# Kernel optimization log

Hardware: AMD Instinct MI355X
Metric: run time of the kernel (lower is better)

The kernel has to match this reference:

```python
import jax, jax.numpy as jnp
from jax import lax
import numpy as np

H = 128; L = 4; N_TOTAL = 4096; M = 4; S = 16384; K = 12; SK = S * K
MAX_DIST = 32; B = 64; NH = 4; DH = H // NH; BN_EPS = 1e-5


def _bn(x, g, b):
    # training-mode BatchNorm1d over rows (biased variance)
    mu = x.mean(0)
    var = x.var(0)
    return (x - mu) * lax.rsqrt(var + BN_EPS) * g + b


def _gine(x, src, dst, ea, eps, We, bWe, W1, b1, W2, b2):
    # PyG GINEConv: mlp((1+eps)*x + sum_j relu(x_j + lin(e_ji)))
    msg = jax.nn.relu(x[src] + ea @ We.T + bWe)
    agg = jax.ops.segment_sum(msg, dst, num_segments=x.shape[0])
    h = (1.0 + eps) * x + agg
    return jax.nn.relu(h @ W1.T + b1) @ W2.T + b2


def _forward(log_probs, atom_tab, bond_tab, dist_tab, logp_W, logp_b, lw, lb,
             bn_g, bn_b, eps, mha_in_W, mha_in_b, mha_out_W, mha_out_b, ro_g, ro_b,
             atom_ids, node_ids, intra_ei, intra_bond_ids, edge_index, canon_bond_ids, batch):
    sub_batch = jnp.arange(SK, dtype=jnp.int32) // K
    root_flat = jnp.arange(S, dtype=jnp.int32) * K
    valid_f = (node_ids >= 0).astype(jnp.float32)[:, None]
    clamped = jnp.maximum(node_ids, 0)
    x_flat = atom_tab[atom_ids][clamped]            # [SK, H]
    ea_flat = bond_tab[intra_bond_ids]              # [E_intra, H]
    edge_attr = bond_tab[canon_bond_ids]            # [E_canon, H]
    src, dst = intra_ei[0], intra_ei[1]

    # BFS distances from subgraph roots (min-plus relaxation, MAX_DIST sweeps)
    d0 = jnp.full((SK,), MAX_DIST, jnp.int32).at[root_flat].set(0)
    dist = lax.fori_loop(0, MAX_DIST, lambda i, d: d.at[dst].min(d[src] + 1), d0)
    dist = jnp.minimum(dist, MAX_DIST)
    dist_pe = dist_tab[dist]

    logp_pe = jax.nn.relu(log_probs[sub_batch][:, None] @ logp_W.T + logp_b)
    h = (x_flat + dist_pe + logp_pe) * valid_f

    is_root_f = jnp.zeros((SK, 1), jnp.float32).at[root_flat].set(1.0)
    root_ids = node_ids[root_flat]                  # canonical id of each root (>=0)
    cnt = jnp.maximum(jax.ops.segment_sum(jnp.ones((S,), jnp.float32), root_ids,
                                          num_segments=N_TOTAL), 1.0)

    for l in range(L):
        W = lw[l]; bv = lb[l]
        h1 = _gine(h, src, dst, ea_flat, eps[l, 0], W[0], bv[0], W[1], bv[1], W[2], bv[2])
        h1 = _bn(h1, bn_g[l, 0], bn_b[l, 0]) * valid_f
        h_root_b = h[sub_batch * K]
        h_nr = h @ W[3].T + bv[3] + h_root_b @ W[4].T + bv[4]
        h_can = jax.ops.segment_sum(h[root_flat], root_ids, num_segments=N_TOTAL) / cnt[:, None]
        h_int = _gine(h_can, edge_index[0], edge_index[1], edge_attr, eps[l, 1],
                      W[5], bv[5], W[6], bv[6], W[7], bv[7])
        h_int = _bn(h_int, bn_g[l, 1], bn_b[l, 1])
        h_ib = h_int[clamped] * valid_f
        out = is_root_f * (h1 + h_ib) + (1.0 - is_root_f) * (h1 + h_nr)
        h = jax.nn.relu(out) * valid_f

    # subgraph sum-pool (invalid rows are zeroed so scatter of zeros is a no-op)
    h_sub = jax.ops.segment_sum(h * valid_f, sub_batch, num_segments=S)
    order = jnp.argsort(root_ids)                   # stable by default
    h2 = h_sub[order].reshape(N_TOTAL, M, H)

    # MultiheadAttention over the m subgraphs of each canonical node
    qkv = h2 @ mha_in_W.T + mha_in_b
    q, k_, v = jnp.split(qkv, 3, axis=-1)
    hd = lambda t: t.reshape(N_TOTAL, M, NH, DH).transpose(0, 2, 1, 3)
    q, k_, v = hd(q), hd(k_), hd(v)
    scale = np.float32(1.0 / np.sqrt(DH))
    attn = jax.nn.softmax(jnp.einsum('nhqd,nhkd->nhqk', q, k_) * scale, axis=-1)
    o = jnp.einsum('nhqk,nhkd->nhqd', attn, v).transpose(0, 2, 1, 3).reshape(N_TOTAL, M, H)
    h_attn = o @ mha_out_W.T + mha_out_b + h2
    node_emb = _bn(h_attn.mean(1), ro_g, ro_b)
    return jax.ops.segment_sum(node_emb, batch, num_segments=B)


def setup_inputs() -> dict:
    key = jax.random.key(0)
    ks = jax.random.split(key, 32)
    rn = lambda i, sh, sc=0.1: (jax.random.normal(ks[i], sh) * sc).astype(jnp.float32)
    atom_ids = jax.random.randint(ks[0], (N_TOTAL,), 0, 64, dtype=jnp.int32)
    nid = jax.random.randint(ks[1], (S, K), 0, N_TOTAL, dtype=jnp.int32)
    pad = jax.random.uniform(ks[2], (S, K)) < 0.1
    nid = jnp.where(pad, -1, nid)
    nid = nid.at[:, 0].set(jnp.arange(S, dtype=jnp.int32) // M)  # roots: each canonical node m times
    node_ids = nid.reshape(-1)
    flat = jnp.arange(SK, dtype=jnp.int32).reshape(S, K)
    intra_ei = jnp.stack([flat[:, :-1].reshape(-1), flat[:, 1:].reshape(-1)])  # chains per subgraph
    intra_bond_ids = jax.random.randint(ks[3], (S * (K - 1),), 0, 8, dtype=jnp.int32)
    edge_index = jax.random.randint(ks[4], (2, N_TOTAL * 8), 0, N_TOTAL, dtype=jnp.int32)
    canon_bond_ids = jax.random.randint(ks[5], (N_TOTAL * 8,), 0, 8, dtype=jnp.int32)
    batch = jnp.arange(N_TOTAL, dtype=jnp.int32) // (N_TOTAL // B)
    log_probs = jax.random.normal(ks[6], (S,), dtype=jnp.float32)
    return dict(
        atom_ids=atom_ids, node_ids=node_ids, intra_ei=intra_ei,
        intra_bond_ids=intra_bond_ids, edge_index=edge_index,
        canon_bond_ids=canon_bond_ids, batch=batch, log_probs=log_probs,
        atom_tab=rn(7, (64, H)), bond_tab=rn(8, (8, H)), dist_tab=rn(9, (MAX_DIST + 1, H)),
        logp_W=rn(10, (H, 1)), logp_b=jnp.zeros((H,), jnp.float32),
        lw=rn(11, (L, 8, H, H)), lb=jnp.zeros((L, 8, H), jnp.float32),
        bn_g=jnp.ones((L, 2, H), jnp.float32), bn_b=jnp.zeros((L, 2, H), jnp.float32),
        eps=jnp.zeros((L, 2), jnp.float32),
        mha_in_W=rn(12, (3 * H, H)), mha_in_b=jnp.zeros((3 * H,), jnp.float32),
        mha_out_W=rn(13, (H, H)), mha_out_b=jnp.zeros((H,), jnp.float32),
        ro_g=jnp.ones((H,), jnp.float32), ro_b=jnp.zeros((H,), jnp.float32))


def reference(atom_ids, node_ids, intra_ei, intra_bond_ids, edge_index, canon_bond_ids,
              batch, log_probs, atom_tab, bond_tab, dist_tab, logp_W, logp_b, lw, lb,
              bn_g, bn_b, eps, mha_in_W, mha_in_b, mha_out_W, mha_out_b, ro_g, ro_b):
    return _forward(log_probs, atom_tab, bond_tab, dist_tab, logp_W, logp_b, lw, lb,
                    bn_g, bn_b, eps, mha_in_W, mha_in_b, mha_out_W, mha_out_b, ro_g, ro_b,
                    atom_ids, node_ids, intra_ei, intra_bond_ids, edge_index, canon_bond_ids, batch)
```

## Files before the change

### kernel.cpp

```cpp
#include <hip/hip_runtime.h>
#include <math.h>

#define DEV static __device__ __forceinline__

constexpr int H    = 128;
constexpr int Ksub = 12;
constexpr int S    = 16384;
constexpr int SK   = S * Ksub;
constexpr int NTOT = 4096;

typedef __attribute__((ext_vector_type(8))) short bhalf8;
typedef __attribute__((ext_vector_type(4))) float floatx4;

DEV float4 ld4(const float* p) { return *(const float4*)p; }
DEV void   st4(float* p, float4 v) { *(float4*)p = v; }

DEV ushort f2b(float f) {
  unsigned x = __float_as_uint(f);
  return (ushort)((x + 0x7FFFu + ((x >> 16) & 1u)) >> 16);
}
DEV float b2f(ushort u) { return __uint_as_float(((unsigned)u) << 16); }

DEV void split8(const float* v, bhalf8& hi, bhalf8& lo) {
#pragma unroll
  for (int j = 0; j < 8; ++j) {
    ushort hv = f2b(v[j]);
    hi[j] = (short)hv;
    lo[j] = (short)f2b(v[j] - b2f(hv));
  }
}


__global__ __launch_bounds__(256) void mm12(
    const float* __restrict__ X,
    const ushort* __restrict__ W1hi, const ushort* __restrict__ W1lo,
    const float* __restrict__ b1,
    const ushort* __restrict__ W2hi, const ushort* __restrict__ W2lo,
    const float* __restrict__ b2, float* __restrict__ Y,
    const float* __restrict__ bp, const int* __restrict__ bid,
    const float* __restrict__ eps_p, float* __restrict__ stats)
{
  __shared__ unsigned int tls[128][132];
  const int tid  = threadIdx.x;
  const int lane = tid & 63, wv = tid >> 6;
  const int wr = (wv >> 1) * 64, wc = (wv & 1) * 64;
  const int m = lane & 15, q = lane >> 4;
  const int row0 = blockIdx.x * 128;
  const float scal = 1.0f + eps_p[0];

  floatx4 acc[4][4];
#pragma unroll
  for (int i = 0; i < 4; ++i)
#pragma unroll
    for (int j = 0; j < 4; ++j) acc[i][j] = (floatx4){0.f, 0.f, 0.f, 0.f};

  size_t arow[4], brow[4];
  int qi[4];
  const float* bprow[4];
#pragma unroll
  for (int i = 0; i < 4; ++i) {
    int grow = row0 + wr + 16 * i + m;
    arow[i] = (size_t)grow * H;
    qi[i] = grow % Ksub;
    bprow[i] = qi[i] ? (bp + (size_t)bid[(grow / Ksub) * (Ksub - 1) + qi[i] - 1] * H)
                     : nullptr;
  }
#pragma unroll
  for (int j = 0; j < 4; ++j) brow[j] = (size_t)(wc + 16 * j + m) * H;

#pragma unroll
  for (int s = 0; s < 4; ++s) {
    const int ko = s * 32 + q * 8;
    bhalf8 bhi[4], blo[4];
#pragma unroll
    for (int j = 0; j < 4; ++j) {
      bhi[j] = *(const bhalf8*)(W1hi + brow[j] + ko);
      blo[j] = *(const bhalf8*)(W1lo + brow[j] + ko);
    }
    bhalf8 ahi[4], alo[4];
#pragma unroll
    for (int i = 0; i < 4; ++i) {
      float xv[8];
      *(float4*)&xv[0] = ld4(X + arow[i] + ko);
      *(float4*)&xv[4] = ld4(X + arow[i] + ko + 4);
      if (qi[i]) {
        float pv[8], bv[8];
        *(float4*)&pv[0] = ld4(X + arow[i] - H + ko);
        *(float4*)&pv[4] = ld4(X + arow[i] - H + ko + 4);
        *(float4*)&bv[0] = ld4(bprow[i] + ko);
        *(float4*)&bv[4] = ld4(bprow[i] + ko + 4);
#pragma unroll
        for (int j = 0; j < 8; ++j)
          xv[j] = fmaf(scal, xv[j], fmaxf(pv[j] + bv[j], 0.f));
      } else {
#pragma unroll
        for (int j = 0; j < 8; ++j) xv[j] *= scal;
      }
      split8(xv, ahi[i], alo[i]);
    }
#pragma unroll
    for (int i = 0; i < 4; ++i)
#pragma unroll
      for (int j = 0; j < 4; ++j) {
        acc[i][j] = __builtin_amdgcn_mfma_f32_16x16x32_bf16(ahi[i], bhi[j], acc[i][j], 0, 0, 0);
        acc[i][j] = __builtin_amdgcn_mfma_f32_16x16x32_bf16(ahi[i], blo[j], acc[i][j], 0, 0, 0);
        acc[i][j] = __builtin_amdgcn_mfma_f32_16x16x32_bf16(alo[i], bhi[j], acc[i][j], 0, 0, 0);
      }
  }

#pragma unroll
  for (int j = 0; j < 4; ++j) {
    const int col = wc + 16 * j + m;
    const float bcol = b1[col];
#pragma unroll
    for (int i = 0; i < 4; ++i) {
      const int lr = wr + 16 * i + 4 * q;
#pragma unroll
      for (int r = 0; r < 4; ++r) {
        float y = fmaxf(acc[i][j][r] + bcol, 0.f);
        ushort hv = f2b(y);
        ushort lv = f2b(y - b2f(hv));
        tls[lr + r][col] = ((unsigned)hv << 16) | lv;
      }
    }
  }
  __syncthreads();

#pragma unroll
  for (int i = 0; i < 4; ++i)
#pragma unroll
    for (int j = 0; j < 4; ++j) acc[i][j] = (floatx4){0.f, 0.f, 0.f, 0.f};

#pragma unroll
  for (int s = 0; s < 4; ++s) {
    const int ko = s * 32 + q * 8;
    bhalf8 bhi[4], blo[4];
#pragma unroll
    for (int j = 0; j < 4; ++j) {
      bhi[j] = *(const bhalf8*)(W2hi + brow[j] + ko);
      blo[j] = *(const bhalf8*)(W2lo + brow[j] + ko);
    }
    bhalf8 ahi[4], alo[4];
#pragma unroll
    for (int i = 0; i < 4; ++i) {
      const int lr = wr + 16 * i + m;
      uint4 u0 = *(const uint4*)&tls[lr][ko];
      uint4 u1 = *(const uint4*)&tls[lr][ko + 4];
      unsigned uu[8] = {u0.x, u0.y, u0.z, u0.w, u1.x, u1.y, u1.z, u1.w};
#pragma unroll
      for (int j = 0; j < 8; ++j) {
        ahi[i][j] = (short)(uu[j] >> 16);
        alo[i][j] = (short)(uu[j] & 0xffffu);
      }
    }
#pragma unroll
    for (int i = 0; i < 4; ++i)
#pragma unroll
      for (int j = 0; j < 4; ++j) {
        acc[i][j] = __builtin_amdgcn_mfma_f32_16x16x32_bf16(ahi[i], bhi[j], acc[i][j], 0, 0, 0);
        acc[i][j] = __builtin_amdgcn_mfma_f32_16x16x32_bf16(ahi[i], blo[j], acc[i][j], 0, 0, 0);
        acc[i][j] = __builtin_amdgcn_mfma_f32_16x16x32_bf16(alo[i], bhi[j], acc[i][j], 0, 0, 0);
      }
  }
  __syncthreads();

  float* sredS = (float*)&tls[0][0];
  float* sredQ = sredS + 1024;
  float psum[4], psq[4];
#pragma unroll
  for (int j = 0; j < 4; ++j) { psum[j] = 0.f; psq[j] = 0.f; }

#pragma unroll
  for (int j = 0; j < 4; ++j) {
    const int col = wc + 16 * j + m;
    const float bcol = b2[col];
#pragma unroll
    for (int i = 0; i < 4; ++i) {
      const int gr = row0 + wr + 16 * i + 4 * q;
#pragma unroll
      for (int r = 0; r < 4; ++r) {
        float y = acc[i][j][r] + bcol;
        Y[(size_t)(gr + r) * H + col] = y;
        psum[j] += y; psq[j] += y * y;
      }
    }
  }
  const int slot = 4 * (wv >> 1) + q;
#pragma unroll
  for (int j = 0; j < 4; ++j) {
    const int col = wc + 16 * j + m;
    sredS[slot * 128 + col] = psum[j];
    sredQ[slot * 128 + col] = psq[j];
  }
  __syncthreads();
  if (tid < 128) {
    float s = 0.f, q2 = 0.f;
#pragma unroll
    for (int t = 0; t < 8; ++t) { s += sredS[t * 128 + tid]; q2 += sredQ[t * 128 + tid]; }
    float* stc = stats + (blockIdx.x & 7) * 256;
    atomicAdd(stc + tid, s);
    atomicAdd(stc + 128 + tid, q2);
  }
}

template<int PRO, int EPI>
__global__ __launch_bounds__(256) void mmN(
    const float* __restrict__ X, const ushort* __restrict__ Whi,
    const ushort* __restrict__ Wlo, const float* __restrict__ bias,
    float* __restrict__ Y,
    const float* __restrict__ a1, const float* __restrict__ a2,
    const float* __restrict__ a3, const int* __restrict__ ids,
    float* __restrict__ stats, const float* __restrict__ bng,
    const float* __restrict__ bnb,
    const float* __restrict__ stats2, const float* __restrict__ bng2,
    const float* __restrict__ bnb2, const float* __restrict__ eps_p,
    float invR, float invR2, size_t ybstride)
{
  __shared__ float sred[2][8][128];
  const int tid  = threadIdx.x;
  const int lane = tid & 63, wv = tid >> 6;
  const int wr = (wv >> 1) * 64, wc = (wv & 1) * 64;
  const int m = lane & 15, q = lane >> 4;
  const int row0 = blockIdx.x * 128;
  const int yb = blockIdx.y;
  Whi  += (size_t)yb * (H * H);
  Wlo  += (size_t)yb * (H * H);
  bias += yb * H;
  Y    += (size_t)yb * ybstride;

  float scal = 1.0f;
  if (PRO == 1) scal = 1.0f + eps_p[0];

  floatx4 acc[4][4];
#pragma unroll
  for (int i = 0; i < 4; ++i)
#pragma unroll
    for (int j = 0; j < 4; ++j) acc[i][j] = (floatx4){0.f, 0.f, 0.f, 0.f};

  size_t arow[4], brow[4];
#pragma unroll
  for (int i = 0; i < 4; ++i) {
    int grow = row0 + wr + 16 * i + m;
    arow[i] = (size_t)(PRO == 2 ? grow * Ksub : grow) * H;
  }
#pragma unroll
  for (int j = 0; j < 4; ++j) brow[j] = (size_t)(wc + 16 * j + m) * H;

  float xv[2][4][8];
#define STAGE_A(SS, BUF)                                                     \
  {                                                                          \
    const int ko_ = (SS) * 32 + q * 8;                                       \
    _Pragma("unroll")                                                        \
    for (int ii = 0; ii < 4; ++ii) {                                         \
      *(float4*)&BUF[ii][0] = ld4(X + arow[ii] + ko_);                       \
      *(float4*)&BUF[ii][4] = ld4(X + arow[ii] + ko_ + 4);                   \
      if (PRO == 1) {                                                        \
        float av_[8];                                                        \
        *(float4*)&av_[0] = ld4(a1 + arow[ii] + ko_);                        \
        *(float4*)&av_[4] = ld4(a1 + arow[ii] + ko_ + 4);                    \
        _Pragma("unroll")                                                    \
        for (int jj = 0; jj < 8; ++jj)                                       \
          BUF[ii][jj] = fmaf(scal, BUF[ii][jj], av_[jj]);                    \
      }                                                                      \
    }                                                                        \
  }

  STAGE_A(0, xv[0]);
#pragma unroll
  for (int s = 0; s < 4; ++s) {
    if (s < 3) STAGE_A(s + 1, xv[(s + 1) & 1]);
    const int ko = s * 32 + q * 8;
    bhalf8 bhi[4], blo[4];
#pragma unroll
    for (int j = 0; j < 4; ++j) {
      bhi[j] = *(const bhalf8*)(Whi + brow[j] + ko);
      blo[j] = *(const bhalf8*)(Wlo + brow[j] + ko);
    }
    bhalf8 ahi[4], alo[4];
#pragma unroll
    for (int i = 0; i < 4; ++i) split8(xv[s & 1][i], ahi[i], alo[i]);
#pragma unroll
    for (int i = 0; i < 4; ++i)
#pragma unroll
      for (int j = 0; j < 4; ++j) {
        acc[i][j] = __builtin_amdgcn_mfma_f32_16x16x32_bf16(ahi[i], bhi[j], acc[i][j], 0, 0, 0);
        acc[i][j] = __builtin_amdgcn_mfma_f32_16x16x32_bf16(ahi[i], blo[j], acc[i][j], 0, 0, 0);
        acc[i][j] = __builtin_amdgcn_mfma_f32_16x16x32_bf16(alo[i], bhi[j], acc[i][j], 0, 0, 0);
      }
  }
#undef STAGE_A

  __syncthreads();

  float psum[4], psq[4];
#pragma unroll
  for (int j = 0; j < 4; ++j) { psum[j] = 0.f; psq[j] = 0.f; }

#pragma unroll
  for (int j = 0; j < 4; ++j) {
    const int col = wc + 16 * j + m;
    const float bcol = bias[col];
    float mu = 0.f, rs = 0.f, gg = 0.f, bb = 0.f;
    float mu2 = 0.f, rs2 = 0.f, gg2 = 0.f, bb2 = 0.f;
    if (EPI == 3) {
      mu = stats[col] * invR;
      rs = rsqrtf(stats[128 + col] * invR - mu * mu + 1e-5f);
      gg = bng[col]; bb = bnb[col];
      mu2 = stats2[col] * invR2;
      rs2 = rsqrtf(stats2[128 + col] * invR2 - mu2 * mu2 + 1e-5f);
      gg2 = bng2[col]; bb2 = bnb2[col];
    }
#pragma unroll
    for (int i = 0; i < 4; ++i) {
      const int rowb = row0 + wr + 16 * i + 4 * q;
#pragma unroll
      for (int r = 0; r < 4; ++r) {
        const int gr = rowb + r;
        float y = acc[i][j][r] + bcol;
        if (EPI == 1) y = fmaxf(y, 0.f);
        if (EPI == 4) y += a1[(size_t)gr * H + col];
        if (EPI == 3) {
          int nid = ids[gr];
          float vf = (nid >= 0) ? 1.f : 0.f;
          bool root = (gr % Ksub) == 0;
          float t2v = a1[(size_t)gr * H + col];
          float h1 = fmaf((t2v - mu) * rs, gg, bb);
          float addv;
          if (root) {
            float c3v = a2[(size_t)nid * H + col];
            addv = fmaf((c3v - mu2) * rs2, gg2, bb2);
          } else {
            addv = y + a3[(size_t)(gr / Ksub) * H + col];
          }
          y = vf * fmaxf(h1 + addv, 0.f);
        }
        Y[(size_t)gr * H + col] = y;
        if (EPI == 2) { psum[j] += y; psq[j] += y * y; }
      }
    }
  }

  if (EPI == 2) {
    const int slot = 4 * (wv >> 1) + q;
#pragma unroll
    for (int j = 0; j < 4; ++j) {
      const int col = wc + 16 * j + m;
      sred[0][slot][col] = psum[j];
      sred[1][slot][col] = psq[j];
    }
    __syncthreads();
    if (tid < 128) {
      float s = 0.f, q2 = 0.f;
#pragma unroll
      for (int t = 0; t < 8; ++t) { s += sred[0][t][tid]; q2 += sred[1][t][tid]; }
      float* stc = stats + (blockIdx.x & 7) * 256;
      atomicAdd(stc + tid, s);
      atomicAdd(stc + 128 + tid, q2);
    }
  }
}

__global__ void k_fold(const float* __restrict__ in, float* __restrict__ out) {
  int b = blockIdx.x, c = threadIdx.x;
  const float* p = in + (size_t)b * 2048;
  float s = 0.f;
#pragma unroll
  for (int k = 0; k < 8; ++k) s += p[k * 256 + c];
  out[b * 256 + c] = s;
}

__global__ void k_split(const float* __restrict__ src, ushort* __restrict__ hi,
                        ushort* __restrict__ lo, int n) {
  int i = (blockIdx.x * 256 + threadIdx.x) * 4;
  if (i >= n) return;
  float4 v = ld4(src + i);
  float vv[4] = {v.x, v.y, v.z, v.w};
#pragma unroll
  for (int j = 0; j < 4; ++j) {
    ushort hv = f2b(vv[j]);
    hi[i + j] = hv;
    lo[i + j] = f2b(vv[j] - b2f(hv));
  }
}

__global__ void k_init_h(float* __restrict__ h, const int* __restrict__ node_ids,
                         const int* __restrict__ atom_ids,
                         const float* __restrict__ atom_tab, const float* __restrict__ dist_tab,
                         const float* __restrict__ log_probs, const float* __restrict__ logp_W,
                         const float* __restrict__ logp_b)
{
  int idx = blockIdx.x * 256 + threadIdx.x;
  if (idx >= SK * 32) return;
  int r = idx >> 5, c4 = (idx & 31) * 4;
  int nid = node_ids[r];
  float valid = nid >= 0 ? 1.f : 0.f;
  int cl = nid >= 0 ? nid : 0;
  int aid = atom_ids[cl];
  int dd = r % Ksub;
  float lp = log_probs[r / Ksub];
  float4 at = ld4(atom_tab + aid * H + c4);
  float4 dt = ld4(dist_tab + dd * H + c4);
  float4 w  = ld4(logp_W + c4);
  float4 bbv = ld4(logp_b + c4);
  float4 o;
  o.x = (at.x + dt.x + fmaxf(fmaf(lp, w.x, bbv.x), 0.f)) * valid;
  o.y = (at.y + dt.y + fmaxf(fmaf(lp, w.y, bbv.y), 0.f)) * valid;
  o.z = (at.z + dt.z + fmaxf(fmaf(lp, w.z, bbv.z), 0.f)) * valid;
  o.w = (at.w + dt.w + fmaxf(fmaf(lp, w.w, bbv.w), 0.f)) * valid;
  st4(h + (size_t)r * H + c4, o);
}

__global__ void k_bond_all(const float* __restrict__ bt, const float* __restrict__ lw,
                           const float* __restrict__ lb, float* __restrict__ bp_all)
{
  int mb = blockIdx.x;
  int c = threadIdx.x;
  int l = mb >> 1, wsel = (mb & 1) ? 5 : 0;
  const float* W = lw + ((size_t)l * 8 + wsel) * H * H;
  const float* b = lb + ((size_t)l * 8 + wsel) * H;
  for (int j = 0; j < 8; ++j) {
    float s = b[c];
    for (int k = 0; k < H; ++k) s = fmaf(bt[j * H + k], W[c * H + k], s);
    bp_all[(size_t)(mb * 8 + j) * H + c] = s;
  }
}

__global__ void k_c1(const float* __restrict__ h, float* __restrict__ c1,
                     float* __restrict__ c2f) {
  int idx = blockIdx.x * 256 + threadIdx.x;
  if (idx >= NTOT * 32) return;
  int n = idx >> 5, c4 = (idx & 31) * 4;
  float o0 = 0.f, o1 = 0.f, o2 = 0.f, o3 = 0.f;
#pragma unroll
  for (int mi = 0; mi < 4; ++mi) {
    const float* p = h + ((size_t)(4 * n + mi) * Ksub) * H + c4;
    o0 += p[0]; o1 += p[1]; o2 += p[2]; o3 += p[3];
  }
  st4(c1 + (size_t)n * H + c4, make_float4(o0 * .25f, o1 * .25f, o2 * .25f, o3 * .25f));
  st4(c2f + (size_t)n * H + c4, make_float4(0.f, 0.f, 0.f, 0.f));
}

__global__ void k_agg(const float* __restrict__ x, const int* __restrict__ src,
                      const int* __restrict__ dst, const int* __restrict__ bid,
                      const float* __restrict__ bp, float* __restrict__ out, int E)
{
  int idx = blockIdx.x * 256 + threadIdx.x;
  if (idx >= E * 32) return;
  int e = idx >> 5, c4 = (idx & 31) * 4;
  int sv = src[e], dv = dst[e], bb = bid[e];
  float4 xv = ld4(x + (size_t)sv * H + c4);
  float4 bv = ld4(bp + (size_t)bb * H + c4);
  float* o = out + (size_t)dv * H + c4;
  atomicAdd(o + 0, fmaxf(xv.x + bv.x, 0.f));
  atomicAdd(o + 1, fmaxf(xv.y + bv.y, 0.f));
  atomicAdd(o + 2, fmaxf(xv.z + bv.z, 0.f));
  atomicAdd(o + 3, fmaxf(xv.w + bv.w, 0.f));
}

__global__ void k_pool(const float* __restrict__ h, float* __restrict__ hsub) {
  int idx = blockIdx.x * 256 + threadIdx.x;
  if (idx >= S * 32) return;
  int s = idx >> 5, c4 = (idx & 31) * 4;
  float a0 = 0.f, a1 = 0.f, a2 = 0.f, a3 = 0.f;
  const float* p = h + ((size_t)s * Ksub) * H + c4;
#pragma unroll
  for (int j = 0; j < Ksub; ++j) {
    a0 += p[0]; a1 += p[1]; a2 += p[2]; a3 += p[3];
    p += H;
  }
  st4(hsub + (size_t)s * H + c4, make_float4(a0, a1, a2, a3));
}

__global__ __launch_bounds__(128) void k_attn(const float* __restrict__ qb,
                                              const float* __restrict__ kb,
                                              const float* __restrict__ vb,
                                              float* __restrict__ ob)
{
  int n = blockIdx.x;
  int c = threadIdx.x;
  float q[4], kv[4], vv[4];
#pragma unroll
  for (int mi = 0; mi < 4; ++mi) {
    q[mi]  = qb[(size_t)(n * 4 + mi) * H + c];
    kv[mi] = kb[(size_t)(n * 4 + mi) * H + c];
    vv[mi] = vb[(size_t)(n * 4 + mi) * H + c];
  }
  const float scale = 0.17677669529663687f;
  float sc[4][4];
#pragma unroll
  for (int m1 = 0; m1 < 4; ++m1)
#pragma unroll
    for (int m2 = 0; m2 < 4; ++m2) {
      float p = q[m1] * kv[m2];
#pragma unroll
      for (int off = 16; off > 0; off >>= 1) p += __shfl_xor(p, off, 32);
      sc[m1][m2] = p * scale;
    }
#pragma unroll
  for (int m1 = 0; m1 < 4; ++m1) {
    float mx = fmaxf(fmaxf(sc[m1][0], sc[m1][1]), fmaxf(sc[m1][2], sc[m1][3]));
    float e0 = expf(sc[m1][0] - mx), e1 = expf(sc[m1][1] - mx);
    float e2 = expf(sc[m1][2] - mx), e3 = expf(sc[m1][3] - mx);
    float inv = 1.f / (e0 + e1 + e2 + e3);
    ob[(size_t)(n * 4 + m1) * H + c] =
        (e0 * vv[0] + e1 * vv[1] + e2 * vv[2] + e3 * vv[3]) * inv;
  }
}

__global__ void k_mean(const float* __restrict__ ha, float* __restrict__ ne) {
  int idx = blockIdx.x * 256 + threadIdx.x;
  if (idx >= NTOT * 32) return;
  int n = idx >> 5, c4 = (idx & 31) * 4;
  float4 a = ld4(ha + (size_t)(n * 4 + 0) * H + c4);
  float4 b = ld4(ha + (size_t)(n * 4 + 1) * H + c4);
  float4 c = ld4(ha + (size_t)(n * 4 + 2) * H + c4);
  float4 d = ld4(ha + (size_t)(n * 4 + 3) * H + c4);
  st4(ne + (size_t)n * H + c4,
      make_float4((a.x + b.x + c.x + d.x) * .25f, (a.y + b.y + c.y + d.y) * .25f,
                  (a.z + b.z + c.z + d.z) * .25f, (a.w + b.w + c.w + d.w) * .25f));
}

__global__ __launch_bounds__(256) void k_bn_stats(const float* __restrict__ X, int R,
                                                  float* __restrict__ stats) {
  __shared__ float sh[2][256];
  int c = threadIdx.x & 127;
  int rr = threadIdx.x >> 7;
  float s = 0.f, s2 = 0.f;
  for (int r = blockIdx.x * 2 + rr; r < R; r += gridDim.x * 2) {
    float v = X[(size_t)r * H + c];
    s += v; s2 += v * v;
  }
  sh[0][threadIdx.x] = s; sh[1][threadIdx.x] = s2;
  __syncthreads();
  if (rr == 0) {
    float* stc = stats + (blockIdx.x & 7) * 256;
    atomicAdd(stc + c,       s  + sh[0][threadIdx.x + 128]);
    atomicAdd(stc + 128 + c, s2 + sh[1][threadIdx.x + 128]);
  }
}

__global__ __launch_bounds__(128) void k_finalsum(const float* __restrict__ ne,
                                                  const float* __restrict__ stats,
                                                  const float* __restrict__ g,
                                                  const float* __restrict__ b,
                                                  float* __restrict__ out)
{
  int bg = blockIdx.x;
  int c = threadIdx.x;
  const float invR = 1.0f / (float)NTOT;
  float mu = stats[c] * invR;
  float rs = rsqrtf(stats[128 + c] * invR - mu * mu + 1e-5f);
  float gg = g[c], bb = b[c];
  float acc = 0.f;
  for (int r = 0; r < 64; ++r) {
    float v = ne[(size_t)(bg * 64 + r) * H + c];
    acc += (v - mu) * rs * gg + bb;
  }
  out[(size_t)bg * H + c] = acc;
}

extern "C" void kernel_launch(void* const* d_in, const int* in_sizes, int n_in,
                              void* d_out, int out_size, void* d_ws, size_t ws_size,
                              hipStream_t stream)
{
  const int*   atom_ids   = (const int*)d_in[0];
  const int*   node_ids   = (const int*)d_in[1];
  const int*   intra_bid  = (const int*)d_in[3];
  const int*   edge_index = (const int*)d_in[4];
  const int*   canon_bid  = (const int*)d_in[5];
  const float* log_probs  = (const float*)d_in[7];
  const float* atom_tab   = (const float*)d_in[8];
  const float* bond_tab   = (const float*)d_in[9];
  const float* dist_tab   = (const float*)d_in[10];
  const float* logp_W     = (const float*)d_in[11];
  const float* logp_b     = (const float*)d_in[12];
  const float* lw         = (const float*)d_in[13];
  const float* lb         = (const float*)d_in[14];
  const float* bn_g       = (const float*)d_in[15];
  const float* bn_b       = (const float*)d_in[16];
  const float* eps        = (const float*)d_in[17];
  const float* mha_in_W   = (const float*)d_in[18];
  const float* mha_in_b   = (const float*)d_in[19];
  const float* mha_out_W  = (const float*)d_in[20];
  const float* mha_out_b  = (const float*)d_in[21];
  const float* ro_g       = (const float*)d_in[22];
  const float* ro_b       = (const float*)d_in[23];

  const int E2 = in_sizes[4] / 2;
  const int* src2 = edge_index, *dst2 = edge_index + E2;

  const size_t SKH = (size_t)SK * H;
  char* wsb = (char*)d_ws;
  float*  h      = (float*)wsb;     wsb += SKH * 4;
  float*  t      = (float*)wsb;     wsb += SKH * 4;
  float*  rproj  = (float*)wsb;     wsb += (size_t)S * H * 4;
  float*  c1     = (float*)wsb;     wsb += (size_t)NTOT * H * 4;
  float*  c2b    = (float*)wsb;     wsb += (size_t)NTOT * H * 4;
  float*  c3     = (float*)wsb;     wsb += (size_t)NTOT * H * 4;
  float*  c2f    = (float*)wsb;     wsb += (size_t)NTOT * H * 4;
  float*  bp_all = (float*)wsb;     wsb += (size_t)64 * H * 4;
  float*  statsA = (float*)wsb;     wsb += 9 * 2048 * 4;
  float*  statsF = (float*)wsb;     wsb += 9 * 256 * 4;
  ushort* lwhi   = (ushort*)wsb;    wsb += (size_t)4 * 8 * H * H * 2;
  ushort* lwlo   = (ushort*)wsb;    wsb += (size_t)4 * 8 * H * H * 2;
  ushort* mihi   = (ushort*)wsb;    wsb += (size_t)3 * H * H * 2;
  ushort* milo   = (ushort*)wsb;    wsb += (size_t)3 * H * H * 2;
  ushort* mohi   = (ushort*)wsb;    wsb += (size_t)H * H * 2;
  ushort* molo   = (ushort*)wsb;    wsb += (size_t)H * H * 2;
  float* hsub = t;
  float* qkv  = hsub + (size_t)S * H;
  float* ob   = qkv + 3 * (size_t)S * H;
  float* ne   = ob + (size_t)S * H;
  float* out  = (float*)d_out;

  hipMemsetAsync(statsA, 0, 9 * 2048 * sizeof(float), stream);
  const int NLW = 4 * 8 * H * H, NMI = 3 * H * H, NMO = H * H;
  k_split<<<(NLW / 4 + 255) / 256, 256, 0, stream>>>(lw, lwhi, lwlo, NLW);
  k_split<<<(NMI / 4 + 255) / 256, 256, 0, stream>>>(mha_in_W, mihi, milo, NMI);
  k_split<<<(NMO / 4 + 255) / 256, 256, 0, stream>>>(mha_out_W, mohi, molo, NMO);
  k_bond_all<<<8, 128, 0, stream>>>(bond_tab, lw, lb, bp_all);
  k_init_h<<<(SK * 32 + 255) / 256, 256, 0, stream>>>(h, node_ids, atom_ids,
      atom_tab, dist_tab, log_probs, logp_W, logp_b);

  for (int l = 0; l < 4; ++l) {
    const ushort* Whi = lwhi + (size_t)l * 8 * H * H;
    const ushort* Wlo = lwlo + (size_t)l * 8 * H * H;
    const float* bb = lb + (size_t)l * 8 * H;
    const float* g0 = bn_g + (l * 2 + 0) * H, *b0  = bn_b + (l * 2 + 0) * H;
    const float* g1 = bn_g + (l * 2 + 1) * H, *b1v = bn_b + (l * 2 + 1) * H;
    const float* eps0 = eps + l * 2, *eps1 = eps + l * 2 + 1;
    float* st0raw = statsA + (size_t)(2 * l + 0) * 2048;
    float* st1raw = statsA + (size_t)(2 * l + 1) * 2048;
    float* st0 = statsF + (size_t)l * 512;
    float* st1 = statsF + (size_t)l * 512 + 256;
    const float* bp0 = bp_all + (size_t)(l * 2 + 0) * 8 * H;
    const float* bp1 = bp_all + (size_t)(l * 2 + 1) * 8 * H;

    mm12<<<SK / 128, 256, 0, stream>>>(h, Whi + 1 * H * H, Wlo + 1 * H * H, bb + 1 * H,
        Whi + 2 * H * H, Wlo + 2 * H * H, bb + 2 * H, t, bp0, intra_bid, eps0, st0raw);
    mmN<2, 0><<<dim3(S / 128, 1), 256, 0, stream>>>(h, Whi + 4 * H * H, Wlo + 4 * H * H,
        bb + 4 * H, rproj, nullptr, nullptr, nullptr, nullptr, nullptr, nullptr, nullptr,
        nullptr, nullptr, nullptr, nullptr, 0.f, 0.f, 0);
    k_c1<<<(NTOT * 32 + 255) / 256, 256, 0, stream>>>(h, c1, c2f);
    k_agg<<<(E2 * 32 + 255) / 256, 256, 0, stream>>>(c1, src2, dst2, canon_bid, bp1, c2f, E2);
    mmN<1, 1><<<dim3(NTOT / 128, 1), 256, 0, stream>>>(c1, Whi + 6 * H * H, Wlo + 6 * H * H,
        bb + 6 * H, c2b, c2f, nullptr, nullptr, nullptr, nullptr, nullptr, nullptr,
        nullptr, nullptr, nullptr, eps1, 0.f, 0.f, 0);
    mmN<0, 2><<<dim3(NTOT / 128, 1), 256, 0, stream>>>(c2b, Whi + 7 * H * H, Wlo + 7 * H * H,
        bb + 7 * H, c3, nullptr, nullptr, nullptr, nullptr, st1raw, nullptr, nullptr,
        nullptr, nullptr, nullptr, nullptr, 0.f, 0.f, 0);
    k_fold<<<2, 256, 0, stream>>>(st0raw, st0);
    mmN<0, 3><<<dim3(SK / 128, 1), 256, 0, stream>>>(h, Whi + 3 * H * H, Wlo + 3 * H * H,
        bb + 3 * H, h, t, c3, rproj, node_ids, st0, g0, b0, st1, g1, b1v, nullptr,
        1.0f / (float)SK, 1.0f / (float)NTOT, 0);
  }

  k_pool<<<(S * 32 + 255) / 256, 256, 0, stream>>>(h, hsub);
  mmN<0, 0><<<dim3(S / 128, 3), 256, 0, stream>>>(hsub, mihi, milo, mha_in_b, qkv,
      nullptr, nullptr, nullptr, nullptr, nullptr, nullptr, nullptr, nullptr, nullptr,
      nullptr, nullptr, 0.f, 0.f, (size_t)S * H);
  k_attn<<<NTOT, 128, 0, stream>>>(qkv, qkv + (size_t)S * H, qkv + 2 * (size_t)S * H, ob);
  mmN<0, 4><<<dim3(S / 128, 1), 256, 0, stream>>>(ob, mohi, molo, mha_out_b, ob,
      hsub, nullptr, nullptr, nullptr, nullptr, nullptr, nullptr, nullptr, nullptr,
      nullptr, nullptr, 0.f, 0.f, 0);
  k_mean<<<(NTOT * 32 + 255) / 256, 256, 0, stream>>>(ob, ne);
  float* stFraw = statsA + (size_t)8 * 2048;
  float* stF    = statsF + (size_t)4 * 512;
  k_bn_stats<<<512, 256, 0, stream>>>(ne, NTOT, stFraw);
  k_fold<<<1, 256, 0, stream>>>(stFraw, stF);
  k_finalsum<<<64, 128, 0, stream>>>(ne, stF, ro_g, ro_b, out);
}
```

Before: 1.632 ms.

## Store activations as pre-split bf16 hi/lo pairs and unfuse the two-GEMM MLP

Large activation buffers (h, t, qkv, attention output) are now kept as separate bf16 hi and lo arrays instead of fp32. GEMMs can feed MFMA directly without splitting each tile on load, and the split happens once at store time. The fused mm12 kernel is replaced by two mmD launches that round-trip the intermediate through global memory. The striped stats atomics and the k_fold kernels are also dropped in favour of direct atomics. In exchange there is an extra kernel launch and an extra intermediate write/read per layer, and atomic contention on the stats grows.

```diff
diff --git a/kernel.cpp b/kernel.cpp
--- a/kernel.cpp
+++ b/kernel.cpp
@@ -21,6 +21,15 @@
 }
 DEV float b2f(ushort u) { return __uint_as_float(((unsigned)u) << 16); }
 
+DEV void st_hl(ushort* hi, ushort* lo, float v) {
+  ushort h = f2b(v);
+  *hi = h;
+  *lo = f2b(v - b2f(h));
+}
+DEV float ld_hl(const ushort* hi, const ushort* lo) {
+  return b2f(*hi) + b2f(*lo);
+}
+
 DEV void split8(const float* v, bhalf8& hi, bhalf8& lo) {
 #pragma unroll
   for (int j = 0; j < 8; ++j) {
@@ -30,191 +39,20 @@
   }
 }
 
-
-__global__ __launch_bounds__(256) void mm12(
-    const float* __restrict__ X,
-    const ushort* __restrict__ W1hi, const ushort* __restrict__ W1lo,
-    const float* __restrict__ b1,
-    const ushort* __restrict__ W2hi, const ushort* __restrict__ W2lo,
-    const float* __restrict__ b2, float* __restrict__ Y,
-    const float* __restrict__ bp, const int* __restrict__ bid,
-    const float* __restrict__ eps_p, float* __restrict__ stats)
-{
-  __shared__ unsigned int tls[128][132];
-  const int tid  = threadIdx.x;
-  const int lane = tid & 63, wv = tid >> 6;
-  const int wr = (wv >> 1) * 64, wc = (wv & 1) * 64;
-  const int m = lane & 15, q = lane >> 4;
-  const int row0 = blockIdx.x * 128;
-  const float scal = 1.0f + eps_p[0];
-
-  floatx4 acc[4][4];
-#pragma unroll
-  for (int i = 0; i < 4; ++i)
-#pragma unroll
-    for (int j = 0; j < 4; ++j) acc[i][j] = (floatx4){0.f, 0.f, 0.f, 0.f};
-
-  size_t arow[4], brow[4];
-  int qi[4];
-  const float* bprow[4];
-#pragma unroll
-  for (int i = 0; i < 4; ++i) {
-    int grow = row0 + wr + 16 * i + m;
-    arow[i] = (size_t)grow * H;
-    qi[i] = grow % Ksub;
-    bprow[i] = qi[i] ? (bp + (size_t)bid[(grow / Ksub) * (Ksub - 1) + qi[i] - 1] * H)
-                     : nullptr;
-  }
-#pragma unroll
-  for (int j = 0; j < 4; ++j) brow[j] = (size_t)(wc + 16 * j + m) * H;
-
-#pragma unroll
-  for (int s = 0; s < 4; ++s) {
-    const int ko = s * 32 + q * 8;
-    bhalf8 bhi[4], blo[4];
-#pragma unroll
-    for (int j = 0; j < 4; ++j) {
-      bhi[j] = *(const bhalf8*)(W1hi + brow[j] + ko);
-      blo[j] = *(const bhalf8*)(W1lo + brow[j] + ko);
-    }
-    bhalf8 ahi[4], alo[4];
-#pragma unroll
-    for (int i = 0; i < 4; ++i) {
-      float xv[8];
-      *(float4*)&xv[0] = ld4(X + arow[i] + ko);
-      *(float4*)&xv[4] = ld4(X + arow[i] + ko + 4);
-      if (qi[i]) {
-        float pv[8], bv[8];
-        *(float4*)&pv[0] = ld4(X + arow[i] - H + ko);
-        *(float4*)&pv[4] = ld4(X + arow[i] - H + ko + 4);
-        *(float4*)&bv[0] = ld4(bprow[i] + ko);
-        *(float4*)&bv[4] = ld4(bprow[i] + ko + 4);
-#pragma unroll
-        for (int j = 0; j < 8; ++j)
-          xv[j] = fmaf(scal, xv[j], fmaxf(pv[j] + bv[j], 0.f));
-      } else {
-#pragma unroll
-        for (int j = 0; j < 8; ++j) xv[j] *= scal;
-      }
-      split8(xv, ahi[i], alo[i]);
-    }
-#pragma unroll
-    for (int i = 0; i < 4; ++i)
-#pragma unroll
-      for (int j = 0; j < 4; ++j) {
-        acc[i][j] = __builtin_amdgcn_mfma_f32_16x16x32_bf16(ahi[i], bhi[j], acc[i][j], 0, 0, 0);
-        acc[i][j] = __builtin_amdgcn_mfma_f32_16x16x32_bf16(ahi[i], blo[j], acc[i][j], 0, 0, 0);
-        acc[i][j] = __builtin_amdgcn_mfma_f32_16x16x32_bf16(alo[i], bhi[j], acc[i][j], 0, 0, 0);
-      }
-  }
-
-#pragma unroll
-  for (int j = 0; j < 4; ++j) {
-    const int col = wc + 16 * j + m;
-    const float bcol = b1[col];
-#pragma unroll
-    for (int i = 0; i < 4; ++i) {
-      const int lr = wr + 16 * i + 4 * q;
-#pragma unroll
-      for (int r = 0; r < 4; ++r) {
-        float y = fmaxf(acc[i][j][r] + bcol, 0.f);
-        ushort hv = f2b(y);
-        ushort lv = f2b(y - b2f(hv));
-        tls[lr + r][col] = ((unsigned)hv << 16) | lv;
-      }
-    }
-  }
-  __syncthreads();
-
-#pragma unroll
-  for (int i = 0; i < 4; ++i)
-#pragma unroll
-    for (int j = 0; j < 4; ++j) acc[i][j] = (floatx4){0.f, 0.f, 0.f, 0.f};
-
-#pragma unroll
-  for (int s = 0; s < 4; ++s) {
-    const int ko = s * 32 + q * 8;
-    bhalf8 bhi[4], blo[4];
-#pragma unroll
-    for (int j = 0; j < 4; ++j) {
-      bhi[j] = *(const bhalf8*)(W2hi + brow[j] + ko);
-      blo[j] = *(const bhalf8*)(W2lo + brow[j] + ko);
-    }
-    bhalf8 ahi[4], alo[4];
-#pragma unroll
-    for (int i = 0; i < 4; ++i) {
-      const int lr = wr + 16 * i + m;
-      uint4 u0 = *(const uint4*)&tls[lr][ko];
-      uint4 u1 = *(const uint4*)&tls[lr][ko + 4];
-      unsigned uu[8] = {u0.x, u0.y, u0.z, u0.w, u1.x, u1.y, u1.z, u1.w};
-#pragma unroll
-      for (int j = 0; j < 8; ++j) {
-        ahi[i][j] = (short)(uu[j] >> 16);
-        alo[i][j] = (short)(uu[j] & 0xffffu);
-      }
-    }
-#pragma unroll
-    for (int i = 0; i < 4; ++i)
-#pragma unroll
-      for (int j = 0; j < 4; ++j) {
-        acc[i][j] = __builtin_amdgcn_mfma_f32_16x16x32_bf16(ahi[i], bhi[j], acc[i][j], 0, 0, 0);
-        acc[i][j] = __builtin_amdgcn_mfma_f32_16x16x32_bf16(ahi[i], blo[j], acc[i][j], 0, 0, 0);
-        acc[i][j] = __builtin_amdgcn_mfma_f32_16x16x32_bf16(alo[i], bhi[j], acc[i][j], 0, 0, 0);
-      }
-  }
-  __syncthreads();
-
-  float* sredS = (float*)&tls[0][0];
-  float* sredQ = sredS + 1024;
-  float psum[4], psq[4];
-#pragma unroll
-  for (int j = 0; j < 4; ++j) { psum[j] = 0.f; psq[j] = 0.f; }
-
-#pragma unroll
-  for (int j = 0; j < 4; ++j) {
-    const int col = wc + 16 * j + m;
-    const float bcol = b2[col];
-#pragma unroll
-    for (int i = 0; i < 4; ++i) {
-      const int gr = row0 + wr + 16 * i + 4 * q;
-#pragma unroll
-      for (int r = 0; r < 4; ++r) {
-        float y = acc[i][j][r] + bcol;
-        Y[(size_t)(gr + r) * H + col] = y;
-        psum[j] += y; psq[j] += y * y;
-      }
-    }
-  }
-  const int slot = 4 * (wv >> 1) + q;
-#pragma unroll
-  for (int j = 0; j < 4; ++j) {
-    const int col = wc + 16 * j + m;
-    sredS[slot * 128 + col] = psum[j];
-    sredQ[slot * 128 + col] = psq[j];
-  }
-  __syncthreads();
-  if (tid < 128) {
-    float s = 0.f, q2 = 0.f;
-#pragma unroll
-    for (int t = 0; t < 8; ++t) { s += sredS[t * 128 + tid]; q2 += sredQ[t * 128 + tid]; }
-    float* stc = stats + (blockIdx.x & 7) * 256;
-    atomicAdd(stc + tid, s);
-    atomicAdd(stc + 128 + tid, q2);
-  }
-}
-
 template<int PRO, int EPI>
-__global__ __launch_bounds__(256) void mmN(
-    const float* __restrict__ X, const ushort* __restrict__ Whi,
-    const ushort* __restrict__ Wlo, const float* __restrict__ bias,
-    float* __restrict__ Y,
-    const float* __restrict__ a1, const float* __restrict__ a2,
-    const float* __restrict__ a3, const int* __restrict__ ids,
+__global__ __launch_bounds__(256) void mmD(
+    const ushort* __restrict__ Xhi, const ushort* __restrict__ Xlo,
+    const ushort* __restrict__ Whi, const ushort* __restrict__ Wlo,
+    const float* __restrict__ bias,
+    ushort* __restrict__ Yhi, ushort* __restrict__ Ylo, float* __restrict__ Yf,
+    const ushort* __restrict__ a1hi, const ushort* __restrict__ a1lo,
+    const float* __restrict__ bpf, const int* __restrict__ ids,
+    const float* __restrict__ a2, const float* __restrict__ a3,
     float* __restrict__ stats, const float* __restrict__ bng,
     const float* __restrict__ bnb,
     const float* __restrict__ stats2, const float* __restrict__ bng2,
     const float* __restrict__ bnb2, const float* __restrict__ eps_p,
-    float invR, float invR2, size_t ybstride)
+    float invR, float invR2, size_t ybstr)
 {
   __shared__ float sred[2][8][128];
   const int tid  = threadIdx.x;
@@ -226,10 +64,11 @@
   Whi  += (size_t)yb * (H * H);
   Wlo  += (size_t)yb * (H * H);
   bias += yb * H;
-  Y    += (size_t)yb * ybstride;
+  Yhi  += (size_t)yb * ybstr;
+  Ylo  += (size_t)yb * ybstr;
 
   float scal = 1.0f;
-  if (PRO == 1) scal = 1.0f + eps_p[0];
+  if (PRO == 3) scal = 1.0f + eps_p[0];
 
   floatx4 acc[4][4];
 #pragma unroll
@@ -238,47 +77,60 @@
     for (int j = 0; j < 4; ++j) acc[i][j] = (floatx4){0.f, 0.f, 0.f, 0.f};
 
   size_t arow[4], brow[4];
+  int qi[4] = {0, 0, 0, 0};
+  const float* bprow[4] = {nullptr, nullptr, nullptr, nullptr};
 #pragma unroll
   for (int i = 0; i < 4; ++i) {
     int grow = row0 + wr + 16 * i + m;
     arow[i] = (size_t)(PRO == 2 ? grow * Ksub : grow) * H;
+    if (PRO == 3) {
+      qi[i] = grow % Ksub;
+      if (qi[i]) bprow[i] = bpf + (size_t)ids[(grow / Ksub) * (Ksub - 1) + qi[i] - 1] * H;
+    }
   }
 #pragma unroll
   for (int j = 0; j < 4; ++j) brow[j] = (size_t)(wc + 16 * j + m) * H;
 
-  float xv[2][4][8];
-#define STAGE_A(SS, BUF)                                                     \
-  {                                                                          \
-    const int ko_ = (SS) * 32 + q * 8;                                       \
-    _Pragma("unroll")                                                        \
-    for (int ii = 0; ii < 4; ++ii) {                                         \
-      *(float4*)&BUF[ii][0] = ld4(X + arow[ii] + ko_);                       \
-      *(float4*)&BUF[ii][4] = ld4(X + arow[ii] + ko_ + 4);                   \
-      if (PRO == 1) {                                                        \
-        float av_[8];                                                        \
-        *(float4*)&av_[0] = ld4(a1 + arow[ii] + ko_);                        \
-        *(float4*)&av_[4] = ld4(a1 + arow[ii] + ko_ + 4);                    \
-        _Pragma("unroll")                                                    \
-        for (int jj = 0; jj < 8; ++jj)                                       \
-          BUF[ii][jj] = fmaf(scal, BUF[ii][jj], av_[jj]);                    \
-      }                                                                      \
-    }                                                                        \
-  }
-
-  STAGE_A(0, xv[0]);
 #pragma unroll
   for (int s = 0; s < 4; ++s) {
-    if (s < 3) STAGE_A(s + 1, xv[(s + 1) & 1]);
     const int ko = s * 32 + q * 8;
+    bhalf8 ahi[4], alo[4];
+#pragma unroll
+    for (int i = 0; i < 4; ++i) {
+      if (PRO == 3) {
+        bhalf8 xh = *(const bhalf8*)(Xhi + arow[i] + ko);
+        bhalf8 xl = *(const bhalf8*)(Xlo + arow[i] + ko);
+        float xv[8];
+#pragma unroll
+        for (int j = 0; j < 8; ++j)
+          xv[j] = b2f((ushort)xh[j]) + b2f((ushort)xl[j]);
+        if (qi[i]) {
+          bhalf8 ph = *(const bhalf8*)(Xhi + arow[i] - H + ko);
+          bhalf8 pl = *(const bhalf8*)(Xlo + arow[i] - H + ko);
+          float bv[8];
+          *(float4*)&bv[0] = ld4(bprow[i] + ko);
+          *(float4*)&bv[4] = ld4(bprow[i] + ko + 4);
+#pragma unroll
+          for (int j = 0; j < 8; ++j) {
+            float pv = b2f((ushort)ph[j]) + b2f((ushort)pl[j]);
+            xv[j] = fmaf(scal, xv[j], fmaxf(pv + bv[j], 0.f));
+          }
+        } else {
+#pragma unroll
+          for (int j = 0; j < 8; ++j) xv[j] *= scal;
+        }
+        split8(xv, ahi[i], alo[i]);
+      } else {
+        ahi[i] = *(const bhalf8*)(Xhi + arow[i] + ko);
+        alo[i] = *(const bhalf8*)(Xlo + arow[i] + ko);
+      }
+    }
     bhalf8 bhi[4], blo[4];
 #pragma unroll
     for (int j = 0; j < 4; ++j) {
       bhi[j] = *(const bhalf8*)(Whi + brow[j] + ko);
       blo[j] = *(const bhalf8*)(Wlo + brow[j] + ko);
     }
-    bhalf8 ahi[4], alo[4];
-#pragma unroll
-    for (int i = 0; i < 4; ++i) split8(xv[s & 1][i], ahi[i], alo[i]);
 #pragma unroll
     for (int i = 0; i < 4; ++i)
 #pragma unroll
@@ -288,7 +140,6 @@
         acc[i][j] = __builtin_amdgcn_mfma_f32_16x16x32_bf16(alo[i], bhi[j], acc[i][j], 0, 0, 0);
       }
   }
-#undef STAGE_A
 
   __syncthreads();
 
@@ -316,14 +167,14 @@
 #pragma unroll
       for (int r = 0; r < 4; ++r) {
         const int gr = rowb + r;
+        const size_t off = (size_t)gr * H + col;
         float y = acc[i][j][r] + bcol;
         if (EPI == 1) y = fmaxf(y, 0.f);
-        if (EPI == 4) y += a1[(size_t)gr * H + col];
         if (EPI == 3) {
           int nid = ids[gr];
           float vf = (nid >= 0) ? 1.f : 0.f;
           bool root = (gr % Ksub) == 0;
-          float t2v = a1[(size_t)gr * H + col];
+          float t2v = b2f(a1hi[off]) + b2f(a1lo[off]);
           float h1 = fmaf((t2v - mu) * rs, gg, bb);
           float addv;
           if (root) {
@@ -334,7 +185,14 @@
           }
           y = vf * fmaxf(h1 + addv, 0.f);
         }
-        Y[(size_t)gr * H + col] = y;
+        if (EPI == 4) {
+          y += b2f(a1hi[off]) + b2f(a1lo[off]);
+          Yf[off] = y;
+        } else if (EPI == 5) {
+          Yf[off] = y;
+        } else {
+          st_hl(Yhi + off, Ylo + off, y);
+        }
         if (EPI == 2) { psum[j] += y; psq[j] += y * y; }
       }
     }
@@ -353,20 +211,114 @@
       float s = 0.f, q2 = 0.f;
 #pragma unroll
       for (int t = 0; t < 8; ++t) { s += sred[0][t][tid]; q2 += sred[1][t][tid]; }
-      float* stc = stats + (blockIdx.x & 7) * 256;
-      atomicAdd(stc + tid, s);
-      atomicAdd(stc + 128 + tid, q2);
-    }
-  }
-}
-
-__global__ void k_fold(const float* __restrict__ in, float* __restrict__ out) {
-  int b = blockIdx.x, c = threadIdx.x;
-  const float* p = in + (size_t)b * 2048;
-  float s = 0.f;
-#pragma unroll
-  for (int k = 0; k < 8; ++k) s += p[k * 256 + c];
-  out[b * 256 + c] = s;
+      atomicAdd(stats + tid, s);
+      atomicAdd(stats + 128 + tid, q2);
+    }
+  }
+}
+
+template<int PRO, int EPI>
+__global__ __launch_bounds__(256) void mmF(
+    const float* __restrict__ X, const ushort* __restrict__ Whi,
+    const ushort* __restrict__ Wlo, const float* __restrict__ bias,
+    float* __restrict__ Y, const float* __restrict__ a1,
+    float* __restrict__ stats, const float* __restrict__ eps_p)
+{
+  __shared__ float sred[2][8][128];
+  const int tid  = threadIdx.x;
+  const int lane = tid & 63, wv = tid >> 6;
+  const int wr = (wv >> 1) * 64, wc = (wv & 1) * 64;
+  const int m = lane & 15, q = lane >> 4;
+  const int row0 = blockIdx.x * 128;
+
+  float scal = 1.0f;
+  if (PRO == 1) scal = 1.0f + eps_p[0];
+
+  floatx4 acc[4][4];
+#pragma unroll
+  for (int i = 0; i < 4; ++i)
+#pragma unroll
+    for (int j = 0; j < 4; ++j) acc[i][j] = (floatx4){0.f, 0.f, 0.f, 0.f};
+
+  size_t arow[4], brow[4];
+#pragma unroll
+  for (int i = 0; i < 4; ++i) arow[i] = (size_t)(row0 + wr + 16 * i + m) * H;
+#pragma unroll
+  for (int j = 0; j < 4; ++j) brow[j] = (size_t)(wc + 16 * j + m) * H;
+
+#pragma unroll
+  for (int s = 0; s < 4; ++s) {
+    const int ko = s * 32 + q * 8;
+    bhalf8 bhi[4], blo[4];
+#pragma unroll
+    for (int j = 0; j < 4; ++j) {
+      bhi[j] = *(const bhalf8*)(Whi + brow[j] + ko);
+      blo[j] = *(const bhalf8*)(Wlo + brow[j] + ko);
+    }
+    bhalf8 ahi[4], alo[4];
+#pragma unroll
+    for (int i = 0; i < 4; ++i) {
+      float xv[8];
+      *(float4*)&xv[0] = ld4(X + arow[i] + ko);
+      *(float4*)&xv[4] = ld4(X + arow[i] + ko + 4);
+      if (PRO == 1) {
+        float av[8];
+        *(float4*)&av[0] = ld4(a1 + arow[i] + ko);
+        *(float4*)&av[4] = ld4(a1 + arow[i] + ko + 4);
+#pragma unroll
+        for (int j = 0; j < 8; ++j) xv[j] = fmaf(scal, xv[j], av[j]);
+      }
+      split8(xv, ahi[i], alo[i]);
+    }
+#pragma unroll
+    for (int i = 0; i < 4; ++i)
+#pragma unroll
+      for (int j = 0; j < 4; ++j) {
+        acc[i][j] = __builtin_amdgcn_mfma_f32_16x16x32_bf16(ahi[i], bhi[j], acc[i][j], 0, 0, 0);
+        acc[i][j] = __builtin_amdgcn_mfma_f32_16x16x32_bf16(ahi[i], blo[j], acc[i][j], 0, 0, 0);
+        acc[i][j] = __builtin_amdgcn_mfma_f32_16x16x32_bf16(alo[i], bhi[j], acc[i][j], 0, 0, 0);
+      }
+  }
+
+  __syncthreads();
+
+  float psum[4], psq[4];
+#pragma unroll
+  for (int j = 0; j < 4; ++j) { psum[j] = 0.f; psq[j] = 0.f; }
+
+#pragma unroll
+  for (int j = 0; j < 4; ++j) {
+    const int col = wc + 16 * j + m;
+    const float bcol = bias[col];
+#pragma unroll
+    for (int i = 0; i < 4; ++i) {
+      const int rowb = row0 + wr + 16 * i + 4 * q;
+#pragma unroll
+      for (int r = 0; r < 4; ++r) {
+        float y = acc[i][j][r] + bcol;
+        if (EPI == 1) y = fmaxf(y, 0.f);
+        Y[(size_t)(rowb + r) * H + col] = y;
+        if (EPI == 2) { psum[j] += y; psq[j] += y * y; }
+      }
+    }
+  }
+  if (EPI == 2) {
+    const int slot = 4 * (wv >> 1) + q;
+#pragma unroll
+    for (int j = 0; j < 4; ++j) {
+      const int col = wc + 16 * j + m;
+      sred[0][slot][col] = psum[j];
+      sred[1][slot][col] = psq[j];
+    }
+    __syncthreads();
+    if (tid < 128) {
+      float s = 0.f, q2 = 0.f;
+#pragma unroll
+      for (int t = 0; t < 8; ++t) { s += sred[0][t][tid]; q2 += sred[1][t][tid]; }
+      atomicAdd(stats + tid, s);
+      atomicAdd(stats + 128 + tid, q2);
+    }
+  }
 }
 
 __global__ void k_split(const float* __restrict__ src, ushort* __restrict__ hi,
@@ -376,15 +328,11 @@
   float4 v = ld4(src + i);
   float vv[4] = {v.x, v.y, v.z, v.w};
 #pragma unroll
-  for (int j = 0; j < 4; ++j) {
-    ushort hv = f2b(vv[j]);
-    hi[i + j] = hv;
-    lo[i + j] = f2b(vv[j] - b2f(hv));
-  }
-}
-
-__global__ void k_init_h(float* __restrict__ h, const int* __restrict__ node_ids,
-                         const int* __restrict__ atom_ids,
+  for (int j = 0; j < 4; ++j) st_hl(hi + i + j, lo + i + j, vv[j]);
+}
+
+__global__ void k_init_h(ushort* __restrict__ hhi, ushort* __restrict__ hlo,
+                         const int* __restrict__ node_ids, const int* __restrict__ atom_ids,
                          const float* __restrict__ atom_tab, const float* __restrict__ dist_tab,
                          const float* __restrict__ log_probs, const float* __restrict__ logp_W,
                          const float* __restrict__ logp_b)
@@ -402,12 +350,14 @@
   float4 dt = ld4(dist_tab + dd * H + c4);
   float4 w  = ld4(logp_W + c4);
   float4 bbv = ld4(logp_b + c4);
-  float4 o;
-  o.x = (at.x + dt.x + fmaxf(fmaf(lp, w.x, bbv.x), 0.f)) * valid;
-  o.y = (at.y + dt.y + fmaxf(fmaf(lp, w.y, bbv.y), 0.f)) * valid;
-  o.z = (at.z + dt.z + fmaxf(fmaf(lp, w.z, bbv.z), 0.f)) * valid;
-  o.w = (at.w + dt.w + fmaxf(fmaf(lp, w.w, bbv.w), 0.f)) * valid;
-  st4(h + (size_t)r * H + c4, o);
+  float o[4];
+  o[0] = (at.x + dt.x + fmaxf(fmaf(lp, w.x, bbv.x), 0.f)) * valid;
+  o[1] = (at.y + dt.y + fmaxf(fmaf(lp, w.y, bbv.y), 0.f)) * valid;
+  o[2] = (at.z + dt.z + fmaxf(fmaf(lp, w.z, bbv.z), 0.f)) * valid;
+  o[3] = (at.w + dt.w + fmaxf(fmaf(lp, w.w, bbv.w), 0.f)) * valid;
+  size_t off = (size_t)r * H + c4;
+#pragma unroll
+  for (int j = 0; j < 4; ++j) st_hl(hhi + off + j, hlo + off + j, o[j]);
 }
 
 __global__ void k_bond_all(const float* __restrict__ bt, const float* __restrict__ lw,
@@ -425,18 +375,19 @@
   }
 }
 
-__global__ void k_c1(const float* __restrict__ h, float* __restrict__ c1,
-                     float* __restrict__ c2f) {
+__global__ void k_c1(const ushort* __restrict__ hhi, const ushort* __restrict__ hlo,
+                     float* __restrict__ c1, float* __restrict__ c2f) {
   int idx = blockIdx.x * 256 + threadIdx.x;
   if (idx >= NTOT * 32) return;
   int n = idx >> 5, c4 = (idx & 31) * 4;
-  float o0 = 0.f, o1 = 0.f, o2 = 0.f, o3 = 0.f;
+  float o[4] = {0.f, 0.f, 0.f, 0.f};
 #pragma unroll
   for (int mi = 0; mi < 4; ++mi) {
-    const float* p = h + ((size_t)(4 * n + mi) * Ksub) * H + c4;
-    o0 += p[0]; o1 += p[1]; o2 += p[2]; o3 += p[3];
-  }
-  st4(c1 + (size_t)n * H + c4, make_float4(o0 * .25f, o1 * .25f, o2 * .25f, o3 * .25f));
+    size_t off = ((size_t)(4 * n + mi) * Ksub) * H + c4;
+#pragma unroll
+    for (int j = 0; j < 4; ++j) o[j] += ld_hl(hhi + off + j, hlo + off + j);
+  }
+  st4(c1 + (size_t)n * H + c4, make_float4(o[0] * .25f, o[1] * .25f, o[2] * .25f, o[3] * .25f));
   st4(c2f + (size_t)n * H + c4, make_float4(0.f, 0.f, 0.f, 0.f));
 }
 
@@ -457,33 +408,39 @@
   atomicAdd(o + 3, fmaxf(xv.w + bv.w, 0.f));
 }
 
-__global__ void k_pool(const float* __restrict__ h, float* __restrict__ hsub) {
+__global__ void k_pool(const ushort* __restrict__ hhi, const ushort* __restrict__ hlo,
+                       ushort* __restrict__ shi, ushort* __restrict__ slo) {
   int idx = blockIdx.x * 256 + threadIdx.x;
   if (idx >= S * 32) return;
   int s = idx >> 5, c4 = (idx & 31) * 4;
-  float a0 = 0.f, a1 = 0.f, a2 = 0.f, a3 = 0.f;
-  const float* p = h + ((size_t)s * Ksub) * H + c4;
+  float a[4] = {0.f, 0.f, 0.f, 0.f};
+  size_t off = ((size_t)s * Ksub) * H + c4;
 #pragma unroll
   for (int j = 0; j < Ksub; ++j) {
-    a0 += p[0]; a1 += p[1]; a2 += p[2]; a3 += p[3];
-    p += H;
-  }
-  st4(hsub + (size_t)s * H + c4, make_float4(a0, a1, a2, a3));
-}
-
-__global__ __launch_bounds__(128) void k_attn(const float* __restrict__ qb,
-                                              const float* __restrict__ kb,
-                                              const float* __restrict__ vb,
-                                              float* __restrict__ ob)
+#pragma unroll
+    for (int k = 0; k < 4; ++k) a[k] += ld_hl(hhi + off + k, hlo + off + k);
+    off += H;
+  }
+  size_t so = (size_t)s * H + c4;
+#pragma unroll
+  for (int k = 0; k < 4; ++k) st_hl(shi + so + k, slo + so + k, a[k]);
+}
+
+__global__ __launch_bounds__(128) void k_attn(const ushort* __restrict__ qkhi,
+                                              const ushort* __restrict__ qklo,
+                                              ushort* __restrict__ ohi,
+                                              ushort* __restrict__ olo)
 {
   int n = blockIdx.x;
   int c = threadIdx.x;
+  const size_t SH = (size_t)S * H;
   float q[4], kv[4], vv[4];
 #pragma unroll
   for (int mi = 0; mi < 4; ++mi) {
-    q[mi]  = qb[(size_t)(n * 4 + mi) * H + c];
-    kv[mi] = kb[(size_t)(n * 4 + mi) * H + c];
-    vv[mi] = vb[(size_t)(n * 4 + mi) * H + c];
+    size_t off = (size_t)(n * 4 + mi) * H + c;
+    q[mi]  = ld_hl(qkhi + off, qklo + off);
+    kv[mi] = ld_hl(qkhi + SH + off, qklo + SH + off);
+    vv[mi] = ld_hl(qkhi + 2 * SH + off, qklo + 2 * SH + off);
   }
   const float scale = 0.17677669529663687f;
   float sc[4][4];
@@ -502,8 +459,9 @@
     float e0 = expf(sc[m1][0] - mx), e1 = expf(sc[m1][1] - mx);
     float e2 = expf(sc[m1][2] - mx), e3 = expf(sc[m1][3] - mx);
     float inv = 1.f / (e0 + e1 + e2 + e3);
-    ob[(size_t)(n * 4 + m1) * H + c] =
-        (e0 * vv[0] + e1 * vv[1] + e2 * vv[2] + e3 * vv[3]) * inv;
+    float o = (e0 * vv[0] + e1 * vv[1] + e2 * vv[2] + e3 * vv[3]) * inv;
+    size_t off = (size_t)(n * 4 + m1) * H + c;
+    st_hl(ohi + off, olo + off, o);
   }
 }
 
@@ -533,9 +491,8 @@
   sh[0][threadIdx.x] = s; sh[1][threadIdx.x] = s2;
   __syncthreads();
   if (rr == 0) {
-    float* stc = stats + (blockIdx.x & 7) * 256;
-    atomicAdd(stc + c,       s  + sh[0][threadIdx.x + 128]);
-    atomicAdd(stc + 128 + c, s2 + sh[1][threadIdx.x + 128]);
+    atomicAdd(&stats[c],       s  + sh[0][threadIdx.x + 128]);
+    atomicAdd(&stats[128 + c], s2 + sh[1][threadIdx.x + 128]);
   }
 }
 
@@ -590,16 +547,18 @@
   const int* src2 = edge_index, *dst2 = edge_index + E2;
 
   const size_t SKH = (size_t)SK * H;
+  const size_t SH  = (size_t)S * H;
   char* wsb = (char*)d_ws;
-  float*  h      = (float*)wsb;     wsb += SKH * 4;
-  float*  t      = (float*)wsb;     wsb += SKH * 4;
-  float*  rproj  = (float*)wsb;     wsb += (size_t)S * H * 4;
+  ushort* hhi    = (ushort*)wsb;    wsb += SKH * 2;
+  ushort* hlo    = (ushort*)wsb;    wsb += SKH * 2;
+  ushort* thi    = (ushort*)wsb;    wsb += SKH * 2;
+  ushort* tlo    = (ushort*)wsb;    wsb += SKH * 2;
+  float*  rproj  = (float*)wsb;     wsb += SH * 4;
   float*  c1     = (float*)wsb;     wsb += (size_t)NTOT * H * 4;
   float*  c2b    = (float*)wsb;     wsb += (size_t)NTOT * H * 4;
   float*  c3     = (float*)wsb;     wsb += (size_t)NTOT * H * 4;
   float*  c2f    = (float*)wsb;     wsb += (size_t)NTOT * H * 4;
   float*  bp_all = (float*)wsb;     wsb += (size_t)64 * H * 4;
-  float*  statsA = (float*)wsb;     wsb += 9 * 2048 * 4;
   float*  statsF = (float*)wsb;     wsb += 9 * 256 * 4;
   ushort* lwhi   = (ushort*)wsb;    wsb += (size_t)4 * 8 * H * H * 2;
   ushort* lwlo   = (ushort*)wsb;    wsb += (size_t)4 * 8 * H * H * 2;
@@ -607,19 +566,20 @@
   ushort* milo   = (ushort*)wsb;    wsb += (size_t)3 * H * H * 2;
   ushort* mohi   = (ushort*)wsb;    wsb += (size_t)H * H * 2;
   ushort* molo   = (ushort*)wsb;    wsb += (size_t)H * H * 2;
-  float* hsub = t;
-  float* qkv  = hsub + (size_t)S * H;
-  float* ob   = qkv + 3 * (size_t)S * H;
-  float* ne   = ob + (size_t)S * H;
-  float* out  = (float*)d_out;
-
-  hipMemsetAsync(statsA, 0, 9 * 2048 * sizeof(float), stream);
+  float*  ao     = (float*)wsb;     wsb += SH * 4;
+  float*  ne     = (float*)wsb;     wsb += (size_t)NTOT * H * 4;
+  ushort* shi  = thi;               ushort* slo  = tlo;
+  ushort* qkhi = thi + SH;          ushort* qklo = tlo + SH;
+  ushort* obhi = thi + 4 * SH;      ushort* oblo = tlo + 4 * SH;
+  float* out = (float*)d_out;
+
+  hipMemsetAsync(statsF, 0, 9 * 256 * sizeof(float), stream);
   const int NLW = 4 * 8 * H * H, NMI = 3 * H * H, NMO = H * H;
   k_split<<<(NLW / 4 + 255) / 256, 256, 0, stream>>>(lw, lwhi, lwlo, NLW);
   k_split<<<(NMI / 4 + 255) / 256, 256, 0, stream>>>(mha_in_W, mihi, milo, NMI);
   k_split<<<(NMO / 4 + 255) / 256, 256, 0, stream>>>(mha_out_W, mohi, molo, NMO);
   k_bond_all<<<8, 128, 0, stream>>>(bond_tab, lw, lb, bp_all);
-  k_init_h<<<(SK * 32 + 255) / 256, 256, 0, stream>>>(h, node_ids, atom_ids,
+  k_init_h<<<(SK * 32 + 255) / 256, 256, 0, stream>>>(hhi, hlo, node_ids, atom_ids,
       atom_tab, dist_tab, log_probs, logp_W, logp_b);
 
   for (int l = 0; l < 4; ++l) {
@@ -629,44 +589,44 @@
     const float* g0 = bn_g + (l * 2 + 0) * H, *b0  = bn_b + (l * 2 + 0) * H;
     const float* g1 = bn_g + (l * 2 + 1) * H, *b1v = bn_b + (l * 2 + 1) * H;
     const float* eps0 = eps + l * 2, *eps1 = eps + l * 2 + 1;
-    float* st0raw = statsA + (size_t)(2 * l + 0) * 2048;
-    float* st1raw = statsA + (size_t)(2 * l + 1) * 2048;
     float* st0 = statsF + (size_t)l * 512;
     float* st1 = statsF + (size_t)l * 512 + 256;
     const float* bp0 = bp_all + (size_t)(l * 2 + 0) * 8 * H;
     const float* bp1 = bp_all + (size_t)(l * 2 + 1) * 8 * H;
 
-    mm12<<<SK / 128, 256, 0, stream>>>(h, Whi + 1 * H * H, Wlo + 1 * H * H, bb + 1 * H,
-        Whi + 2 * H * H, Wlo + 2 * H * H, bb + 2 * H, t, bp0, intra_bid, eps0, st0raw);
-    mmN<2, 0><<<dim3(S / 128, 1), 256, 0, stream>>>(h, Whi + 4 * H * H, Wlo + 4 * H * H,
-        bb + 4 * H, rproj, nullptr, nullptr, nullptr, nullptr, nullptr, nullptr, nullptr,
-        nullptr, nullptr, nullptr, nullptr, 0.f, 0.f, 0);
-    k_c1<<<(NTOT * 32 + 255) / 256, 256, 0, stream>>>(h, c1, c2f);
+    mmD<3, 1><<<SK / 128, 256, 0, stream>>>(hhi, hlo, Whi + 1 * H * H, Wlo + 1 * H * H,
+        bb + 1 * H, thi, tlo, nullptr, nullptr, nullptr, bp0, intra_bid,
+        nullptr, nullptr, nullptr, nullptr, nullptr, nullptr, nullptr, nullptr,
+        eps0, 0.f, 0.f, 0);
+    mmD<0, 2><<<SK / 128, 256, 0, stream>>>(thi, tlo, Whi + 2 * H * H, Wlo + 2 * H * H,
+        bb + 2 * H, thi, tlo, nullptr, nullptr, nullptr, nullptr, nullptr,
+        nullptr, nullptr, st0, nullptr, nullptr, nullptr, nullptr, nullptr,
+        nullptr, 0.f, 0.f, 0);
+    mmD<2, 5><<<S / 128, 256, 0, stream>>>(hhi, hlo, Whi + 4 * H * H, Wlo + 4 * H * H,
+        bb + 4 * H, nullptr, nullptr, rproj, nullptr, nullptr, nullptr, nullptr,
+        nullptr, nullptr, nullptr, nullptr, nullptr, nullptr, nullptr, nullptr,
+        nullptr, 0.f, 0.f, 0);
+    k_c1<<<(NTOT * 32 + 255) / 256, 256, 0, stream>>>(hhi, hlo, c1, c2f);
     k_agg<<<(E2 * 32 + 255) / 256, 256, 0, stream>>>(c1, src2, dst2, canon_bid, bp1, c2f, E2);
-    mmN<1, 1><<<dim3(NTOT / 128, 1), 256, 0, stream>>>(c1, Whi + 6 * H * H, Wlo + 6 * H * H,
-        bb + 6 * H, c2b, c2f, nullptr, nullptr, nullptr, nullptr, nullptr, nullptr,
-        nullptr, nullptr, nullptr, eps1, 0.f, 0.f, 0);
-    mmN<0, 2><<<dim3(NTOT / 128, 1), 256, 0, stream>>>(c2b, Whi + 7 * H * H, Wlo + 7 * H * H,
-        bb + 7 * H, c3, nullptr, nullptr, nullptr, nullptr, st1raw, nullptr, nullptr,
-        nullptr, nullptr, nullptr, nullptr, 0.f, 0.f, 0);
-    k_fold<<<2, 256, 0, stream>>>(st0raw, st0);
-    mmN<0, 3><<<dim3(SK / 128, 1), 256, 0, stream>>>(h, Whi + 3 * H * H, Wlo + 3 * H * H,
-        bb + 3 * H, h, t, c3, rproj, node_ids, st0, g0, b0, st1, g1, b1v, nullptr,
-        1.0f / (float)SK, 1.0f / (float)NTOT, 0);
-  }
-
-  k_pool<<<(S * 32 + 255) / 256, 256, 0, stream>>>(h, hsub);
-  mmN<0, 0><<<dim3(S / 128, 3), 256, 0, stream>>>(hsub, mihi, milo, mha_in_b, qkv,
-      nullptr, nullptr, nullptr, nullptr, nullptr, nullptr, nullptr, nullptr, nullptr,
-      nullptr, nullptr, 0.f, 0.f, (size_t)S * H);
-  k_attn<<<NTOT, 128, 0, stream>>>(qkv, qkv + (size_t)S * H, qkv + 2 * (size_t)S * H, ob);
-  mmN<0, 4><<<dim3(S / 128, 1), 256, 0, stream>>>(ob, mohi, molo, mha_out_b, ob,
-      hsub, nullptr, nullptr, nullptr, nullptr, nullptr, nullptr, nullptr, nullptr,
-      nullptr, nullptr, 0.f, 0.f, 0);
-  k_mean<<<(NTOT * 32 + 255) / 256, 256, 0, stream>>>(ob, ne);
-  float* stFraw = statsA + (size_t)8 * 2048;
-  float* stF    = statsF + (size_t)4 * 512;
-  k_bn_stats<<<512, 256, 0, stream>>>(ne, NTOT, stFraw);
-  k_fold<<<1, 256, 0, stream>>>(stFraw, stF);
+    mmF<1, 1><<<NTOT / 128, 256, 0, stream>>>(c1, Whi + 6 * H * H, Wlo + 6 * H * H,
+        bb + 6 * H, c2b, c2f, nullptr, eps1);
+    mmF<0, 2><<<NTOT / 128, 256, 0, stream>>>(c2b, Whi + 7 * H * H, Wlo + 7 * H * H,
+        bb + 7 * H, c3, nullptr, st1, nullptr);
+    mmD<0, 3><<<SK / 128, 256, 0, stream>>>(hhi, hlo, Whi + 3 * H * H, Wlo + 3 * H * H,
+        bb + 3 * H, hhi, hlo, nullptr, thi, tlo, nullptr, node_ids, c3, rproj,
+        st0, g0, b0, st1, g1, b1v, nullptr, 1.0f / (float)SK, 1.0f / (float)NTOT, 0);
+  }
+
+  k_pool<<<(S * 32 + 255) / 256, 256, 0, stream>>>(hhi, hlo, shi, slo);
+  mmD<0, 0><<<dim3(S / 128, 3), 256, 0, stream>>>(shi, slo, mihi, milo, mha_in_b,
+      qkhi, qklo, nullptr, nullptr, nullptr, nullptr, nullptr, nullptr, nullptr,
+      nullptr, nullptr, nullptr, nullptr, nullptr, nullptr, nullptr, 0.f, 0.f, SH);
+  k_attn<<<NTOT, 128, 0, stream>>>(qkhi, qklo, obhi, oblo);
+  mmD<0, 4><<<S / 128, 256, 0, stream>>>(obhi, oblo, mohi, molo, mha_out_b,
+      nullptr, nullptr, ao, shi, slo, nullptr, nullptr, nullptr, nullptr,
+      nullptr, nullptr, nullptr, nullptr, nullptr, nullptr, nullptr, 0.f, 0.f, 0);
+  k_mean<<<(NTOT * 32 + 255) / 256, 256, 0, stream>>>(ao, ne);
+  float* stF = statsF + (size_t)8 * 256;
+  k_bn_stats<<<512, 256, 0, stream>>>(ne, NTOT, stF);
   k_finalsum<<<64, 128, 0, stream>>>(ne, stF, ro_g, ro_b, out);
 }
```

Measured after the change: 1.991 ms. 22.0% more time.
